# Performance work log

Measured on AMD Instinct MI355X. Metric: run time of the kernel, lower is better.

Reference implementation:

```python
import jax, jax.numpy as jnp
import numpy as np

LN_EPS = 1e-12  # BERT LayerNorm eps


def _layernorm(x, g, b):
    mu = jnp.mean(x, axis=-1, keepdims=True)
    var = jnp.mean(jnp.square(x - mu), axis=-1, keepdims=True)
    return (x - mu) * jax.lax.rsqrt(var + LN_EPS) * g + b


def setup_inputs() -> dict:
    key = jax.random.key(0)
    B, M, D, H, dh, R, Ro, Rf, F = 4, 2048, 768, 12, 64, 32, 256, 256, 3072
    ks = iter(jax.random.split(key, 32))
    n = lambda shape, s=0.02: jax.random.normal(next(ks), shape, jnp.float32) * s
    return {
        'x': jax.random.normal(next(ks), (B, M, D), jnp.float32),
        'mask': jnp.zeros((B, M), jnp.float32),  # HF-style additive mask
        'Pq': n((H, D, R)), 'Vq': n((H, R, dh)), 'bq': n((1, H, 1, dh)),
        'Pk': n((H, D, R)), 'Vk': n((H, R, dh)), 'bk': n((1, H, 1, dh)),
        'Pv': n((H, D, R)), 'Vv': n((H, R, dh)), 'bv': n((1, H, 1, dh)),
        'Uo': n((D, Ro)), 'Vo': n((Ro, D)), 'bo_attn': jnp.zeros((D,), jnp.float32),
        'U1': n((D, Rf)), 'V1': n((Rf, F)), 'b1': jnp.zeros((F,), jnp.float32),
        'U2': n((F, Rf)), 'V2': n((Rf, D)), 'b2': jnp.zeros((D,), jnp.float32),
        'ln1_g': jnp.ones((D,), jnp.float32), 'ln1_b': jnp.zeros((D,), jnp.float32),
        'ln2_g': jnp.ones((D,), jnp.float32), 'ln2_b': jnp.zeros((D,), jnp.float32),
    }


def reference(x, mask, Pq, Vq, bq, Pk, Vk, bk, Pv, Vv, bv,
              Uo, Vo, bo_attn, U1, V1, b1, U2, V2, b2,
              ln1_g, ln1_b, ln2_g, ln2_b):
    B, M, D = x.shape
    H, dh = Pq.shape[0], Vq.shape[2]
    # low-rank per-head Q/K/V: x @ P (bhmr) then @ V (bhmd) + bias
    q = jnp.einsum('bhmr,hrd->bhmd', jnp.einsum('bmd,hdr->bhmr', x, Pq), Vq) + bq
    k = jnp.einsum('bhmr,hrd->bhmd', jnp.einsum('bmd,hdr->bhmr', x, Pk), Vk) + bk
    v = jnp.einsum('bhmr,hrd->bhmd', jnp.einsum('bmd,hdr->bhmr', x, Pv), Vv) + bv
    # attention (flash_svd_attention math: scaled dot-product + additive mask)
    scores = jnp.einsum('bhmd,bhnd->bhmn', q, k) / jnp.sqrt(jnp.float32(dh))
    scores = scores + mask[:, None, None, :]
    attn = jnp.einsum('bhmn,bhnd->bhmd', jax.nn.softmax(scores, axis=-1), v)
    attn = attn.transpose(0, 2, 1, 3).reshape(B, M, D)
    # low-rank output projection + residual + LN1
    x1 = _layernorm(x + (attn @ Uo) @ Vo + bo_attn, ln1_g, ln1_b)
    # low-rank FFN (BERT intermediate: exact GELU)
    mid = x1 @ U1
    y = (jax.nn.gelu(mid @ V1 + b1, approximate=False) @ U2) @ V2 + b2
    return _layernorm(x1 + y, ln2_g, ln2_b)
```

## Files before the change

kernel.cpp:

```cpp
#include <hip/hip_runtime.h>
#include <hip/hip_bf16.h>
#include <math.h>

typedef __hip_bfloat16 bf16;
typedef __attribute__((ext_vector_type(8))) short short8;
typedef __attribute__((ext_vector_type(4))) short short4v;
typedef __attribute__((ext_vector_type(4))) float f32x4;

#define C1F 0.18033688011112042f
#define LOG2E 1.44269504088896f

__device__ __forceinline__ float to_f(float x) { return x; }
__device__ __forceinline__ float to_f(bf16 x) { return __bfloat162float(x); }

template <typename T> __device__ __forceinline__ T from_f(float x);
template <> __device__ __forceinline__ float from_f<float>(float x) { return x; }
template <> __device__ __forceinline__ bf16 from_f<bf16>(float x) { return __float2bfloat16(x); }

__device__ __forceinline__ float gelu_exact(float x) {
    return 0.5f * x * (1.0f + erff(x * 0.70710678118654752f));
}

#define GLD_LDS16(g, l)                                               \
    __builtin_amdgcn_global_load_lds(                                 \
        (const __attribute__((address_space(1))) void*)(g),           \
        (__attribute__((address_space(3))) void*)(l), 16, 0, 0)

__global__ __launch_bounds__(256) void build_w_qkv_lds(const float* __restrict__ Pq,
                                                       const float* __restrict__ Vq,
                                                       const float* __restrict__ Pk,
                                                       const float* __restrict__ Vk,
                                                       const float* __restrict__ Pv,
                                                       const float* __restrict__ Vv,
                                                       bf16* __restrict__ Wt) {
    const int dt = blockIdx.x;
    const int h = blockIdx.y;
    const int which = blockIdx.z;
    const float* P = (which == 0) ? Pq : (which == 1) ? Pk : Pv;
    const float* V = (which == 0) ? Vq : (which == 1) ? Vk : Vv;
    const float scale = (which == 0) ? C1F : 1.0f;
    __shared__ __align__(16) float Ps[128][36];
    __shared__ __align__(16) float Vs[32][64];
    __shared__ __align__(16) unsigned int Ot[64][68];
    const int tid = threadIdx.x;

    const float* pbase = P + ((size_t)h * 768 + dt * 128) * 32;
#pragma unroll
    for (int i = 0; i < 4; i++) {
        int idx = tid + i * 256;
        float4 v4 = ((const float4*)pbase)[idx];
        *(float4*)&Ps[idx >> 3][(idx & 7) * 4] = v4;
    }
    const float* vbase = V + (size_t)h * 2048;
#pragma unroll
    for (int i = 0; i < 2; i++) {
        int idx = tid + i * 256;
        ((float4*)&Vs[0][0])[idx] = ((const float4*)vbase)[idx];
    }
    __syncthreads();

    const int e = tid & 63, w = tid >> 6;
    float vreg[32];
#pragma unroll
    for (int r = 0; r < 32; r++) vreg[r] = Vs[r][e];

#pragma unroll
    for (int dp = 0; dp < 16; dp++) {
        const int d0 = w * 32 + dp * 2;
        float a0 = 0.f, a1 = 0.f;
#pragma unroll
        for (int r4 = 0; r4 < 8; r4++) {
            float4 p0 = *(const float4*)&Ps[d0][r4 * 4];
            float4 p1 = *(const float4*)&Ps[d0 + 1][r4 * 4];
            a0 += p0.x * vreg[r4 * 4] + p0.y * vreg[r4 * 4 + 1] + p0.z * vreg[r4 * 4 + 2] + p0.w * vreg[r4 * 4 + 3];
            a1 += p1.x * vreg[r4 * 4] + p1.y * vreg[r4 * 4 + 1] + p1.z * vreg[r4 * 4 + 2] + p1.w * vreg[r4 * 4 + 3];
        }
        a0 *= scale;
        a1 *= scale;
        unsigned int lo = (unsigned int)(unsigned short)__builtin_bit_cast(short, from_f<bf16>(a0));
        unsigned int hi = (unsigned int)(unsigned short)__builtin_bit_cast(short, from_f<bf16>(a1));
        Ot[e][w * 16 + dp] = lo | (hi << 16);
    }
    __syncthreads();

    const int erow = tid >> 2, c0 = (tid & 3) * 16;
    bf16* dst = Wt + ((size_t)which * 768 + h * 64 + erow) * 768 + dt * 128 + c0 * 2;
    *(uint4*)(dst) = *(const uint4*)&Ot[erow][c0];
    *(uint4*)(dst + 8) = *(const uint4*)&Ot[erow][c0 + 4];
    *(uint4*)(dst + 16) = *(const uint4*)&Ot[erow][c0 + 8];
    *(uint4*)(dst + 24) = *(const uint4*)&Ot[erow][c0 + 12];
}

__device__ __forceinline__ void ct_tile(const float* in, bf16* out, int R, int Cc,
                                        int r0, int c0, int tx, int ty) {
    __shared__ float t[32][33];
#pragma unroll
    for (int i = 0; i < 4; i++)
        t[ty + i * 8][tx] = in[(size_t)(r0 + ty + i * 8) * Cc + c0 + tx];
    __syncthreads();
#pragma unroll
    for (int i = 0; i < 4; i++)
        out[(size_t)(c0 + ty + i * 8) * R + r0 + tx] = from_f<bf16>(t[tx][ty + i * 8]);
}

__global__ __launch_bounds__(256) void cast_transpose_t(const float* __restrict__ in,
                                                        bf16* __restrict__ out,
                                                        int R, int Cc) {
    ct_tile(in, out, R, Cc, blockIdx.x * 32, blockIdx.y * 32,
            threadIdx.x & 31, threadIdx.x >> 5);
}

__global__ __launch_bounds__(256) void cast_transpose_batch(const float* __restrict__ U1,
                                                            const float* __restrict__ V1,
                                                            const float* __restrict__ U2,
                                                            const float* __restrict__ V2,
                                                            bf16* __restrict__ U1t,
                                                            bf16* __restrict__ V1t,
                                                            bf16* __restrict__ U2t,
                                                            bf16* __restrict__ V2t) {
    int t = blockIdx.x;
    const float* in;
    bf16* out;
    int R, Cc;
    if (t < 192) { in = U1; out = U1t; R = 768; Cc = 256; }
    else if (t < 960) { t -= 192; in = V1; out = V1t; R = 256; Cc = 3072; }
    else if (t < 1728) { t -= 960; in = U2; out = U2t; R = 3072; Cc = 256; }
    else { t -= 1728; in = V2; out = V2t; R = 256; Cc = 768; }
    const int tpr = Cc >> 5;
    ct_tile(in, out, R, Cc, (t / tpr) * 32, (t % tpr) * 32,
            threadIdx.x & 31, threadIdx.x >> 5);
}

__global__ __launch_bounds__(256) void cast_f32_bf16(const float* __restrict__ in,
                                                     bf16* __restrict__ out, int n4) {
    int t = blockIdx.x * 256 + threadIdx.x;
    if (t >= n4) return;
    float4 v = ((const float4*)in)[t];
    bf16 tmp[4] = {from_f<bf16>(v.x), from_f<bf16>(v.y), from_f<bf16>(v.z), from_f<bf16>(v.w)};
    ((short4v*)out)[t] = *(short4v*)tmp;
}

__global__ __launch_bounds__(256) void pack_bias_mask(const float* __restrict__ bq,
                                                      const float* __restrict__ bk,
                                                      const float* __restrict__ bv,
                                                      const float* __restrict__ mask,
                                                      float* __restrict__ bias_out,
                                                      float* __restrict__ mask2) {
    int t = blockIdx.x * 256 + threadIdx.x;
    if (t < 768) {
        bias_out[t] = bq[t] * C1F;
        bias_out[768 + t] = bk[t];
        bias_out[1536 + t] = bv[t];
    }
    int m = t - 768;
    if (m >= 0 && m < 8192) mask2[m] = mask[m] * LOG2E;
}

template <typename TOUT, int EPI>
__global__ __launch_bounds__(256) void gemm_mfma(const bf16* __restrict__ A,
                                                 const bf16* __restrict__ Bt,
                                                 const float* __restrict__ bias,
                                                 TOUT* __restrict__ C,
                                                 int M, int N, int K) {
    __shared__ __align__(16) bf16 As[128 * 32];
    __shared__ __align__(16) bf16 Bs[128 * 32];
    const int tid = threadIdx.x;
    const int w = tid >> 6, lane = tid & 63;
    const int l = lane & 15, quad = lane >> 4;
    const int wm = w >> 1, wn = w & 1;
    const int m0 = blockIdx.x * 128, n0 = blockIdx.y * 128;

    const int r_in = lane >> 2;
    const int slot = lane & 3;
    const int rA0 = 2 * w * 16 + r_in, rA1 = rA0 + 16;
    const int q0 = slot ^ ((rA0 >> 1) & 3);
    const int q1 = slot ^ ((rA1 >> 1) & 3);
    const bf16* a0 = A + (size_t)(m0 + rA0) * K + q0 * 8;
    const bf16* a1 = A + (size_t)(m0 + rA1) * K + q1 * 8;
    const bf16* b0 = Bt + (size_t)(n0 + rA0) * K + q0 * 8;
    const bf16* b1 = Bt + (size_t)(n0 + rA1) * K + q1 * 8;
    bf16* lA0 = As + 2 * w * 512;
    bf16* lA1 = lA0 + 512;
    bf16* lB0 = Bs + 2 * w * 512;
    bf16* lB1 = lB0 + 512;

    const int swz = (quad ^ ((l >> 1) & 3)) * 8;
    f32x4 acc[4][4] = {};

    for (int k0 = 0; k0 < K; k0 += 32) {
        GLD_LDS16(a0 + k0, lA0);
        GLD_LDS16(a1 + k0, lA1);
        GLD_LDS16(b0 + k0, lB0);
        GLD_LDS16(b1 + k0, lB1);
        __syncthreads();
        short8 af[4], bfr[4];
#pragma unroll
        for (int mt = 0; mt < 4; mt++)
            af[mt] = *(const short8*)&As[(wm * 64 + mt * 16 + l) * 32 + swz];
#pragma unroll
        for (int nt = 0; nt < 4; nt++)
            bfr[nt] = *(const short8*)&Bs[(wn * 64 + nt * 16 + l) * 32 + swz];
#pragma unroll
        for (int mt = 0; mt < 4; mt++)
#pragma unroll
            for (int nt = 0; nt < 4; nt++)
                acc[mt][nt] = __builtin_amdgcn_mfma_f32_16x16x32_bf16(af[mt], bfr[nt], acc[mt][nt], 0, 0, 0);
        __syncthreads();
    }

    float bs[4];
#pragma unroll
    for (int nt = 0; nt < 4; nt++)
        bs[nt] = bias ? bias[n0 + wn * 64 + nt * 16 + l] : 0.f;
#pragma unroll
    for (int mt = 0; mt < 4; mt++) {
#pragma unroll
        for (int nt = 0; nt < 4; nt++) {
            const int col = n0 + wn * 64 + nt * 16 + l;
#pragma unroll
            for (int r = 0; r < 4; r++) {
                const int row = m0 + wm * 64 + mt * 16 + quad * 4 + r;
                float val = acc[mt][nt][r] + bs[nt];
                if (EPI == 1) val = gelu_exact(val);
                C[(size_t)row * N + col] = from_f<TOUT>(val);
            }
        }
    }
}

template <typename TOUT, int EPI>
__global__ __launch_bounds__(256) void gemm_mfma64(const bf16* __restrict__ A,
                                                   const bf16* __restrict__ Bt,
                                                   const float* __restrict__ bias,
                                                   TOUT* __restrict__ C,
                                                   int M, int N, int K) {
    __shared__ __align__(16) bf16 As[64 * 32];
    __shared__ __align__(16) bf16 Bs[64 * 32];
    const int tid = threadIdx.x;
    const int w = tid >> 6, lane = tid & 63;
    const int l = lane & 15, quad = lane >> 4;
    const int wm = w >> 1, wn = w & 1;
    const int m0 = blockIdx.x * 64, n0 = blockIdx.y * 64;

    const int cid = tid;
    const int srow = cid >> 2, slot = cid & 3;
    const int gq = slot ^ ((srow >> 1) & 3);
    const bf16* ag = A + (size_t)(m0 + srow) * K + gq * 8;
    const bf16* bg = Bt + (size_t)(n0 + srow) * K + gq * 8;
    bf16* lA = As + w * 512;
    bf16* lB = Bs + w * 512;

    f32x4 acc[2][2] = {};

    for (int k0 = 0; k0 < K; k0 += 32) {
        GLD_LDS16(ag + k0, lA);
        GLD_LDS16(bg + k0, lB);
        __syncthreads();
        short8 af[2], bfr[2];
#pragma unroll
        for (int mt = 0; mt < 2; mt++) {
            const int row = wm * 32 + mt * 16 + l;
            af[mt] = *(const short8*)&As[row * 32 + (quad ^ ((row >> 1) & 3)) * 8];
        }
#pragma unroll
        for (int nt = 0; nt < 2; nt++) {
            const int row = wn * 32 + nt * 16 + l;
            bfr[nt] = *(const short8*)&Bs[row * 32 + (quad ^ ((row >> 1) & 3)) * 8];
        }
#pragma unroll
        for (int mt = 0; mt < 2; mt++)
#pragma unroll
            for (int nt = 0; nt < 2; nt++)
                acc[mt][nt] = __builtin_amdgcn_mfma_f32_16x16x32_bf16(af[mt], bfr[nt], acc[mt][nt], 0, 0, 0);
        __syncthreads();
    }

#pragma unroll
    for (int mt = 0; mt < 2; mt++) {
#pragma unroll
        for (int nt = 0; nt < 2; nt++) {
            const int col = n0 + wn * 32 + nt * 16 + l;
            const float bsv = bias ? bias[col] : 0.f;
#pragma unroll
            for (int r = 0; r < 4; r++) {
                const int row = m0 + wm * 32 + mt * 16 + quad * 4 + r;
                float val = acc[mt][nt][r] + bsv;
                if (EPI == 1) val = gelu_exact(val);
                C[(size_t)row * N + col] = from_f<TOUT>(val);
            }
        }
    }
}

__global__ __launch_bounds__(256) void transpose_v(const bf16* __restrict__ qkv,
                                                   bf16* __restrict__ vt) {
    __shared__ __align__(16) bf16 t[64][72];
    const int m0 = blockIdx.x * 64;
    const int h = blockIdx.y;
    const int tid = threadIdx.x;
    const int r = tid >> 2, c0 = (tid & 3) * 16;
    {
        const size_t g = (size_t)(m0 + r) * 2304 + 1536 + h * 64 + c0;
        *(short8*)&t[r][c0] = *(const short8*)(qkv + g);
        *(short8*)&t[r][c0 + 8] = *(const short8*)(qkv + g + 8);
    }
    __syncthreads();
    const int b = m0 >> 11, mm = m0 & 2047;
    const int e = tid >> 2, mi0 = (tid & 3) * 16;
    bf16 tmp[16];
#pragma unroll
    for (int j = 0; j < 16; j++) tmp[j] = t[mi0 + j][e];
    bf16* dst = vt + (((size_t)b * 12 + h) * 64 + e) * 2048 + mm + mi0;
    *(short8*)dst = *(short8*)&tmp[0];
    *(short8*)(dst + 8) = *(short8*)&tmp[8];
}

__global__ __launch_bounds__(256, 4) void flash_attn_mfma(const bf16* __restrict__ qkv,
                                                          const bf16* __restrict__ vt,
                                                          const float* __restrict__ mask2,
                                                          bf16* __restrict__ opart0,
                                                          bf16* __restrict__ opart1,
                                                          float* __restrict__ lpart) {
    const int qt = blockIdx.x, h = blockIdx.y;
    const int b = blockIdx.z >> 1, kh = blockIdx.z & 1;
    const int tid = threadIdx.x;
    const int w = tid >> 6, lane = tid & 63;
    const int l = lane & 15, quad = lane >> 4;

    __shared__ __align__(16) bf16 Ks[2][64 * 64];
    __shared__ __align__(16) bf16 Vs[2][64 * 64];
    __shared__ __align__(16) bf16 Ps[4 * 16 * 64];

    short8 qf[2][2];
#pragma unroll
    for (int mt = 0; mt < 2; mt++) {
        const int qrow = qt * 128 + w * 32 + mt * 16 + l;
        const bf16* qp = qkv + ((size_t)b * 2048 + qrow) * 2304 + h * 64 + quad * 8;
        qf[mt][0] = *(const short8*)qp;
        qf[mt][1] = *(const short8*)(qp + 32);
    }

    short8 ones;
#pragma unroll
    for (int i = 0; i < 8; i++) ones[i] = (short)0x3F80;

    f32x4 of[2][4] = {};
    f32x4 lacc[2] = {};
    bf16* Pw = Ps + w * 1024;

    const int kc0 = kh * 1024;
    int cids[2], ldst[2];
    const bf16* kg[2];
    const bf16* vg[2];
#pragma unroll
    for (int i = 0; i < 2; i++) {
        const int cid = (w * 2 + i) * 64 + lane;
        const int row = cid >> 3, slot = cid & 7;
        const int gq = slot ^ (row & 7);
        cids[i] = cid;
        ldst[i] = cid * 8;
        kg[i] = qkv + ((size_t)b * 2048 + kc0 + row) * 2304 + 768 + h * 64 + gq * 8;
        vg[i] = vt + (((size_t)b * 12 + h) * 64 + row) * 2048 + kc0 + gq * 8;
    }
    const float* mp = mask2 + (size_t)b * 2048 + kc0 + quad * 4;

    auto stage = [&](int buf) {
#pragma unroll
        for (int i = 0; i < 2; i++) {
            GLD_LDS16(kg[i], &Ks[buf][ldst[i]]);
            GLD_LDS16(vg[i], &Vs[buf][ldst[i]]);
            kg[i] += 64 * 2304;
            vg[i] += 64;
        }
    };

    int cur = 0;
    stage(0);

#pragma unroll 2
    for (int it = 0; it < 16; it++) {
        __syncthreads();
        float4 mrow[4];
#pragma unroll
        for (int nt = 0; nt < 4; nt++) mrow[nt] = *(const float4*)(mp + nt * 16);
        mp += 64;
        if (it < 15) stage(cur ^ 1);

        const bf16* Kc = Ks[cur];
        const bf16* Vc = Vs[cur];

        f32x4 st[2][4];
#pragma unroll
        for (int nt = 0; nt < 4; nt++) {
            const int rb = (nt * 16 + l) * 64;
            short8 kf0 = *(const short8*)&Kc[rb + ((quad) ^ (l & 7)) * 8];
            short8 kf1 = *(const short8*)&Kc[rb + ((4 + quad) ^ (l & 7)) * 8];
#pragma unroll
            for (int mt = 0; mt < 2; mt++) {
                f32x4 a = {mrow[nt].x, mrow[nt].y, mrow[nt].z, mrow[nt].w};
                a = __builtin_amdgcn_mfma_f32_16x16x32_bf16(kf0, qf[mt][0], a, 0, 0, 0);
                a = __builtin_amdgcn_mfma_f32_16x16x32_bf16(kf1, qf[mt][1], a, 0, 0, 0);
                st[mt][nt] = a;
            }
        }

        short8 pa[2][2];
#pragma unroll
        for (int mt = 0; mt < 2; mt++) {
#pragma unroll
            for (int nt = 0; nt < 4; nt++) {
                float p0 = exp2f(st[mt][nt][0]);
                float p1 = exp2f(st[mt][nt][1]);
                float p2 = exp2f(st[mt][nt][2]);
                float p3 = exp2f(st[mt][nt][3]);
                unsigned d0 = __builtin_amdgcn_perm(__builtin_bit_cast(unsigned, p1),
                                                    __builtin_bit_cast(unsigned, p0), 0x07060302u);
                unsigned d1 = __builtin_amdgcn_perm(__builtin_bit_cast(unsigned, p3),
                                                    __builtin_bit_cast(unsigned, p2), 0x07060302u);
                const int slot8 = (2 * nt + (quad >> 1)) ^ (l & 7);
                uint2 u = {d0, d1};
                *(uint2*)&Pw[l * 64 + slot8 * 8 + (quad & 1) * 4] = u;
            }
#pragma unroll
            for (int ks = 0; ks < 2; ks++)
                pa[mt][ks] = *(const short8*)&Pw[l * 64 + ((ks * 4 + quad) ^ (l & 7)) * 8];
        }

#pragma unroll
        for (int mt = 0; mt < 2; mt++) {
            lacc[mt] = __builtin_amdgcn_mfma_f32_16x16x32_bf16(pa[mt][0], ones, lacc[mt], 0, 0, 0);
            lacc[mt] = __builtin_amdgcn_mfma_f32_16x16x32_bf16(pa[mt][1], ones, lacc[mt], 0, 0, 0);
        }

#pragma unroll
        for (int nt = 0; nt < 4; nt++) {
            const int rb = (nt * 16 + l) * 64;
            short8 vf0 = *(const short8*)&Vc[rb + ((quad) ^ (l & 7)) * 8];
            short8 vf1 = *(const short8*)&Vc[rb + ((4 + quad) ^ (l & 7)) * 8];
#pragma unroll
            for (int mt = 0; mt < 2; mt++) {
                of[mt][nt] = __builtin_amdgcn_mfma_f32_16x16x32_bf16(pa[mt][0], vf0, of[mt][nt], 0, 0, 0);
                of[mt][nt] = __builtin_amdgcn_mfma_f32_16x16x32_bf16(pa[mt][1], vf1, of[mt][nt], 0, 0, 0);
            }
        }
        cur ^= 1;
    }

#pragma unroll
    for (int mt = 0; mt < 2; mt++) {
        if (l == 0) {
#pragma unroll
            for (int r = 0; r < 4; r++)
                lpart[(((size_t)kh * 4 + b) * 12 + h) * 2048 + qt * 128 + w * 32 + mt * 16 + quad * 4 + r] =
                    lacc[mt][r];
        }
    }

    bf16* op = kh ? opart1 : opart0;
#pragma unroll
    for (int mt = 0; mt < 2; mt++) {
#pragma unroll
        for (int r = 0; r < 4; r++) {
            const int row = qt * 128 + w * 32 + mt * 16 + quad * 4 + r;
#pragma unroll
            for (int nt = 0; nt < 4; nt++)
                op[((size_t)b * 2048 + row) * 768 + h * 64 + nt * 16 + l] =
                    from_f<bf16>(of[mt][nt][r]);
        }
    }
}

__global__ __launch_bounds__(256) void attn_combine(const bf16* __restrict__ o0,
                                                    const bf16* __restrict__ o1,
                                                    const float* __restrict__ lp,
                                                    bf16* __restrict__ outp) {
    const int t = blockIdx.x * 256 + threadIdx.x;
    const int col4 = t % 192;
    const int row = t / 192;
    const int b = row >> 11, m = row & 2047;
    const int h = col4 >> 4;
    const float l0 = lp[((size_t)b * 12 + h) * 2048 + m];
    const float l1 = lp[((size_t)(4 + b) * 12 + h) * 2048 + m];
    const float iv = 1.f / (l0 + l1);
    short4v a = ((const short4v*)o0)[t];
    short4v c = ((const short4v*)o1)[t];
    bf16 r[4];
#pragma unroll
    for (int i = 0; i < 4; i++) {
        float f = to_f(__builtin_bit_cast(bf16, a[i])) + to_f(__builtin_bit_cast(bf16, c[i]));
        r[i] = from_f<bf16>(f * iv);
    }
    ((short4v*)outp)[t] = *(short4v*)r;
}

template <typename TIN, typename TADD, typename TOUT>
__global__ __launch_bounds__(256) void ln_kernel(const TIN* __restrict__ base,
                                                 const TADD* __restrict__ add,
                                                 const float* __restrict__ gamma,
                                                 const float* __restrict__ beta,
                                                 TOUT* __restrict__ out) {
    const int row = blockIdx.x;
    const int tid = threadIdx.x;
    __shared__ float red[4];
    const size_t o = (size_t)row * 768;
    float v[3];
#pragma unroll
    for (int i = 0; i < 3; i++) {
        int d = tid + i * 256;
        v[i] = to_f(base[o + d]) + to_f(add[o + d]);
    }
    float s = v[0] + v[1] + v[2];
#pragma unroll
    for (int off = 32; off > 0; off >>= 1) s += __shfl_down(s, off, 64);
    const int wave = tid >> 6, lane = tid & 63;
    if (lane == 0) red[wave] = s;
    __syncthreads();
    float mu = (red[0] + red[1] + red[2] + red[3]) * (1.0f / 768.0f);
    float d0 = v[0] - mu, d1 = v[1] - mu, d2 = v[2] - mu;
    float sq = d0 * d0 + d1 * d1 + d2 * d2;
    __syncthreads();
#pragma unroll
    for (int off = 32; off > 0; off >>= 1) sq += __shfl_down(sq, off, 64);
    if (lane == 0) red[wave] = sq;
    __syncthreads();
    float var = (red[0] + red[1] + red[2] + red[3]) * (1.0f / 768.0f);
    float rs = rsqrtf(var + 1e-12f);
#pragma unroll
    for (int i = 0; i < 3; i++) {
        int d = tid + i * 256;
        float y = (v[i] - mu) * rs * gamma[d] + beta[d];
        out[o + d] = from_f<TOUT>(y);
    }
}

extern "C" void kernel_launch(void* const* d_in, const int* in_sizes, int n_in,
                              void* d_out, int out_size, void* d_ws, size_t ws_size,
                              hipStream_t stream) {
    const float* x    = (const float*)d_in[0];
    const float* mask = (const float*)d_in[1];
    const float* Pq = (const float*)d_in[2];
    const float* Vq = (const float*)d_in[3];
    const float* bq = (const float*)d_in[4];
    const float* Pk = (const float*)d_in[5];
    const float* Vk = (const float*)d_in[6];
    const float* bk = (const float*)d_in[7];
    const float* Pv = (const float*)d_in[8];
    const float* Vv = (const float*)d_in[9];
    const float* bv = (const float*)d_in[10];
    const float* Uo = (const float*)d_in[11];
    const float* Vo = (const float*)d_in[12];
    const float* bo = (const float*)d_in[13];
    const float* U1 = (const float*)d_in[14];
    const float* V1 = (const float*)d_in[15];
    const float* b1 = (const float*)d_in[16];
    const float* U2 = (const float*)d_in[17];
    const float* V2 = (const float*)d_in[18];
    const float* b2 = (const float*)d_in[19];
    const float* g1 = (const float*)d_in[20];
    const float* be1 = (const float*)d_in[21];
    const float* g2 = (const float*)d_in[22];
    const float* be2 = (const float*)d_in[23];

    char* p = (char*)d_ws;
    bf16* Wqkv_t = (bf16*)p;            p += (size_t)2304 * 768 * 2;
    bf16* Wo_t   = (bf16*)p;            p += (size_t)768 * 768 * 2;
    bf16* U1t    = (bf16*)p;            p += (size_t)256 * 768 * 2;
    bf16* V1t    = (bf16*)p;            p += (size_t)3072 * 256 * 2;
    bf16* U2t    = (bf16*)p;            p += (size_t)256 * 3072 * 2;
    bf16* V2t    = (bf16*)p;            p += (size_t)768 * 256 * 2;
    float* bias_qkv = (float*)p;        p += (size_t)2304 * 4;
    float* mask2 = (float*)p;           p += (size_t)8192 * 4;
    bf16* xb     = (bf16*)p;
    bf16* x1b    = xb;                  p += (size_t)8192 * 768 * 2;
    bf16* qkv    = (bf16*)p;
    bf16* gbuf   = qkv;                 p += (size_t)8192 * 2304 * 2;
    bf16* vtb    = (bf16*)p;            p += (size_t)8192 * 768 * 2;
    bf16* attnb  = (bf16*)p;
    bf16* t2     = attnb;               p += (size_t)8192 * 768 * 2;
    char* regR   = p;                   p += (size_t)8192 * 768 * 4;
    bf16* t1     = (bf16*)p;            p += (size_t)8192 * 256 * 2;
    bf16* Vot = (bf16*)regR;
    bf16* Uob = Vot + (size_t)768 * 256;
    bf16* opart1 = (bf16*)regR;
    float* lpart = (float*)(regR + (size_t)8192 * 768 * 2);
    bf16* y1b = (bf16*)regR;
    bf16* y2b = (bf16*)(regR + (size_t)8192 * 768 * 2);

    build_w_qkv_lds<<<dim3(6, 12, 3), 256, 0, stream>>>(Pq, Vq, Pk, Vk, Pv, Vv, Wqkv_t);
    cast_transpose_t<<<dim3(8, 24), 256, 0, stream>>>(Vo, Vot, 256, 768);
    cast_f32_bf16<<<192, 256, 0, stream>>>(Uo, Uob, 768 * 256 / 4);
    gemm_mfma<bf16, 0><<<dim3(6, 6), 256, 0, stream>>>(Vot, Uob, nullptr, Wo_t, 768, 768, 256);
    cast_transpose_batch<<<1920, 256, 0, stream>>>(U1, V1, U2, V2, U1t, V1t, U2t, V2t);
    pack_bias_mask<<<35, 256, 0, stream>>>(bq, bk, bv, mask, bias_qkv, mask2);
    cast_f32_bf16<<<6144, 256, 0, stream>>>(x, xb, 8192 * 768 / 4);

    gemm_mfma<bf16, 0><<<dim3(64, 18), 256, 0, stream>>>(xb, Wqkv_t, bias_qkv, qkv, 8192, 2304, 768);

    transpose_v<<<dim3(128, 12), 256, 0, stream>>>(qkv, vtb);

    flash_attn_mfma<<<dim3(16, 12, 8), 256, 0, stream>>>(qkv, vtb, mask2, attnb, opart1, lpart);
    attn_combine<<<6144, 256, 0, stream>>>(attnb, opart1, lpart, attnb);

    gemm_mfma<bf16, 0><<<dim3(64, 6), 256, 0, stream>>>(attnb, Wo_t, bo, y1b, 8192, 768, 768);

    ln_kernel<bf16, bf16, bf16><<<8192, 256, 0, stream>>>(xb, y1b, g1, be1, x1b);

    gemm_mfma64<bf16, 0><<<dim3(128, 4), 256, 0, stream>>>(x1b, U1t, nullptr, t1, 8192, 256, 768);

    gemm_mfma<bf16, 1><<<dim3(64, 24), 256, 0, stream>>>(t1, V1t, b1, gbuf, 8192, 3072, 256);

    gemm_mfma64<bf16, 0><<<dim3(128, 4), 256, 0, stream>>>(gbuf, U2t, nullptr, t2, 8192, 256, 3072);

    gemm_mfma<bf16, 0><<<dim3(64, 6), 256, 0, stream>>>(t2, V2t, b2, y2b, 8192, 768, 256);

    ln_kernel<bf16, bf16, float><<<8192, 256, 0, stream>>>(x1b, y2b, g2, be2, (float*)d_out);
}
```

Before: 420.9 us.

## Double flash-attention query tile to 256 rows with 512 threads; merge prep casts

```diff
diff --git a/kernel.cpp b/kernel.cpp
--- a/kernel.cpp
+++ b/kernel.cpp
@@ -103,21 +103,16 @@
         out[(size_t)(c0 + ty + i * 8) * R + r0 + tx] = from_f<bf16>(t[tx][ty + i * 8]);
 }
 
-__global__ __launch_bounds__(256) void cast_transpose_t(const float* __restrict__ in,
-                                                        bf16* __restrict__ out,
-                                                        int R, int Cc) {
-    ct_tile(in, out, R, Cc, blockIdx.x * 32, blockIdx.y * 32,
-            threadIdx.x & 31, threadIdx.x >> 5);
-}
-
 __global__ __launch_bounds__(256) void cast_transpose_batch(const float* __restrict__ U1,
                                                             const float* __restrict__ V1,
                                                             const float* __restrict__ U2,
                                                             const float* __restrict__ V2,
+                                                            const float* __restrict__ Vo,
                                                             bf16* __restrict__ U1t,
                                                             bf16* __restrict__ V1t,
                                                             bf16* __restrict__ U2t,
-                                                            bf16* __restrict__ V2t) {
+                                                            bf16* __restrict__ V2t,
+                                                            bf16* __restrict__ Vot) {
     int t = blockIdx.x;
     const float* in;
     bf16* out;
@@ -125,19 +120,27 @@
     if (t < 192) { in = U1; out = U1t; R = 768; Cc = 256; }
     else if (t < 960) { t -= 192; in = V1; out = V1t; R = 256; Cc = 3072; }
     else if (t < 1728) { t -= 960; in = U2; out = U2t; R = 3072; Cc = 256; }
-    else { t -= 1728; in = V2; out = V2t; R = 256; Cc = 768; }
+    else if (t < 1920) { t -= 1728; in = V2; out = V2t; R = 256; Cc = 768; }
+    else { t -= 1920; in = Vo; out = Vot; R = 256; Cc = 768; }
     const int tpr = Cc >> 5;
     ct_tile(in, out, R, Cc, (t / tpr) * 32, (t % tpr) * 32,
             threadIdx.x & 31, threadIdx.x >> 5);
 }
 
-__global__ __launch_bounds__(256) void cast_f32_bf16(const float* __restrict__ in,
-                                                     bf16* __restrict__ out, int n4) {
+__global__ __launch_bounds__(256) void cast_f32_bf16_dual(const float* __restrict__ a,
+                                                          bf16* __restrict__ oa, int n4a,
+                                                          const float* __restrict__ bsrc,
+                                                          bf16* __restrict__ ob, int n4b) {
     int t = blockIdx.x * 256 + threadIdx.x;
-    if (t >= n4) return;
-    float4 v = ((const float4*)in)[t];
+    const float* in;
+    bf16* out;
+    int i;
+    if (t < n4a) { in = a; out = oa; i = t; }
+    else if (t < n4a + n4b) { in = bsrc; out = ob; i = t - n4a; }
+    else return;
+    float4 v = ((const float4*)in)[i];
     bf16 tmp[4] = {from_f<bf16>(v.x), from_f<bf16>(v.y), from_f<bf16>(v.z), from_f<bf16>(v.w)};
-    ((short4v*)out)[t] = *(short4v*)tmp;
+    ((short4v*)out)[i] = *(short4v*)tmp;
 }
 
 __global__ __launch_bounds__(256) void pack_bias_mask(const float* __restrict__ bq,
@@ -315,7 +318,7 @@
     *(short8*)(dst + 8) = *(short8*)&tmp[8];
 }
 
-__global__ __launch_bounds__(256, 4) void flash_attn_mfma(const bf16* __restrict__ qkv,
+__global__ __launch_bounds__(512, 6) void flash_attn_mfma(const bf16* __restrict__ qkv,
                                                           const bf16* __restrict__ vt,
                                                           const float* __restrict__ mask2,
                                                           bf16* __restrict__ opart0,
@@ -329,12 +332,12 @@
 
     __shared__ __align__(16) bf16 Ks[2][64 * 64];
     __shared__ __align__(16) bf16 Vs[2][64 * 64];
-    __shared__ __align__(16) bf16 Ps[4 * 16 * 64];
+    __shared__ __align__(16) bf16 Ps[8 * 16 * 64];
 
     short8 qf[2][2];
 #pragma unroll
     for (int mt = 0; mt < 2; mt++) {
-        const int qrow = qt * 128 + w * 32 + mt * 16 + l;
+        const int qrow = qt * 256 + w * 32 + mt * 16 + l;
         const bf16* qp = qkv + ((size_t)b * 2048 + qrow) * 2304 + h * 64 + quad * 8;
         qf[mt][0] = *(const short8*)qp;
         qf[mt][1] = *(const short8*)(qp + 32);
@@ -349,29 +352,18 @@
     bf16* Pw = Ps + w * 1024;
 
     const int kc0 = kh * 1024;
-    int cids[2], ldst[2];
-    const bf16* kg[2];
-    const bf16* vg[2];
-#pragma unroll
-    for (int i = 0; i < 2; i++) {
-        const int cid = (w * 2 + i) * 64 + lane;
-        const int row = cid >> 3, slot = cid & 7;
-        const int gq = slot ^ (row & 7);
-        cids[i] = cid;
-        ldst[i] = cid * 8;
-        kg[i] = qkv + ((size_t)b * 2048 + kc0 + row) * 2304 + 768 + h * 64 + gq * 8;
-        vg[i] = vt + (((size_t)b * 12 + h) * 64 + row) * 2048 + kc0 + gq * 8;
-    }
+    const int srow = tid >> 3, sslot = tid & 7;
+    const int sgq = sslot ^ (srow & 7);
+    const int ldst = tid * 8;
+    const bf16* kg = qkv + ((size_t)b * 2048 + kc0 + srow) * 2304 + 768 + h * 64 + sgq * 8;
+    const bf16* vg = vt + (((size_t)b * 12 + h) * 64 + srow) * 2048 + kc0 + sgq * 8;
     const float* mp = mask2 + (size_t)b * 2048 + kc0 + quad * 4;
 
     auto stage = [&](int buf) {
-#pragma unroll
-        for (int i = 0; i < 2; i++) {
-            GLD_LDS16(kg[i], &Ks[buf][ldst[i]]);
-            GLD_LDS16(vg[i], &Vs[buf][ldst[i]]);
-            kg[i] += 64 * 2304;
-            vg[i] += 64;
-        }
+        GLD_LDS16(kg, &Ks[buf][ldst]);
+        GLD_LDS16(vg, &Vs[buf][ldst]);
+        kg += 64 * 2304;
+        vg += 64;
     };
 
     int cur = 0;
@@ -451,7 +443,7 @@
         if (l == 0) {
 #pragma unroll
             for (int r = 0; r < 4; r++)
-                lpart[(((size_t)kh * 4 + b) * 12 + h) * 2048 + qt * 128 + w * 32 + mt * 16 + quad * 4 + r] =
+                lpart[(((size_t)kh * 4 + b) * 12 + h) * 2048 + qt * 256 + w * 32 + mt * 16 + quad * 4 + r] =
                     lacc[mt][r];
         }
     }
@@ -461,7 +453,7 @@
     for (int mt = 0; mt < 2; mt++) {
 #pragma unroll
         for (int r = 0; r < 4; r++) {
-            const int row = qt * 128 + w * 32 + mt * 16 + quad * 4 + r;
+            const int row = qt * 256 + w * 32 + mt * 16 + quad * 4 + r;
 #pragma unroll
             for (int nt = 0; nt < 4; nt++)
                 op[((size_t)b * 2048 + row) * 768 + h * 64 + nt * 16 + l] =
@@ -586,19 +578,20 @@
     bf16* y1b = (bf16*)regR;
     bf16* y2b = (bf16*)(regR + (size_t)8192 * 768 * 2);
 
+    constexpr int N4_X = 8192 * 768 / 4;
+    constexpr int N4_UO = 768 * 256 / 4;
+    constexpr int CAST_BLOCKS = (N4_X + N4_UO + 255) / 256;
     build_w_qkv_lds<<<dim3(6, 12, 3), 256, 0, stream>>>(Pq, Vq, Pk, Vk, Pv, Vv, Wqkv_t);
-    cast_transpose_t<<<dim3(8, 24), 256, 0, stream>>>(Vo, Vot, 256, 768);
-    cast_f32_bf16<<<192, 256, 0, stream>>>(Uo, Uob, 768 * 256 / 4);
+    cast_transpose_batch<<<2112, 256, 0, stream>>>(U1, V1, U2, V2, Vo, U1t, V1t, U2t, V2t, Vot);
+    cast_f32_bf16_dual<<<CAST_BLOCKS, 256, 0, stream>>>(x, xb, N4_X, Uo, Uob, N4_UO);
+    pack_bias_mask<<<35, 256, 0, stream>>>(bq, bk, bv, mask, bias_qkv, mask2);
     gemm_mfma<bf16, 0><<<dim3(6, 6), 256, 0, stream>>>(Vot, Uob, nullptr, Wo_t, 768, 768, 256);
-    cast_transpose_batch<<<1920, 256, 0, stream>>>(U1, V1, U2, V2, U1t, V1t, U2t, V2t);
-    pack_bias_mask<<<35, 256, 0, stream>>>(bq, bk, bv, mask, bias_qkv, mask2);
-    cast_f32_bf16<<<6144, 256, 0, stream>>>(x, xb, 8192 * 768 / 4);
 
     gemm_mfma<bf16, 0><<<dim3(64, 18), 256, 0, stream>>>(xb, Wqkv_t, bias_qkv, qkv, 8192, 2304, 768);
 
     transpose_v<<<dim3(128, 12), 256, 0, stream>>>(qkv, vtb);
 
-    flash_attn_mfma<<<dim3(16, 12, 8), 256, 0, stream>>>(qkv, vtb, mask2, attnb, opart1, lpart);
+    flash_attn_mfma<<<dim3(8, 12, 8), 512, 0, stream>>>(qkv, vtb, mask2, attnb, opart1, lpart);
     attn_combine<<<6144, 256, 0, stream>>>(attnb, opart1, lpart, attnb);
 
     gemm_mfma<bf16, 0><<<dim3(64, 6), 256, 0, stream>>>(attnb, Wo_t, bo, y1b, 8192, 768, 768);
```

After: 717.4 us. 1.7x slower.
